# Kernel optimization log

Measured on AMD Instinct MI355X. Metric: run time of the kernel, lower is better.

The kernel has to match this reference:

```python
import jax, jax.numpy as jnp
import numpy as np
from jax import lax

T, D, NH, CATS = 1024, 2048, 2048, 1000


def setup_inputs() -> dict:
    key = jax.random.key(0)
    ks = jax.random.split(key, 16)
    s = 0.02
    return {
        "x": jax.random.normal(ks[0], (T, D), dtype=jnp.float32),
        "Wh": jax.random.normal(ks[1], (NH, D), dtype=jnp.float32) * s,
        "Wz": jax.random.normal(ks[2], (NH, D), dtype=jnp.float32) * s,
        "Wr": jax.random.normal(ks[3], (NH, D), dtype=jnp.float32) * s,
        "Uh": jax.random.normal(ks[4], (NH, NH), dtype=jnp.float32) * s,
        "Uz": jax.random.normal(ks[5], (NH, NH), dtype=jnp.float32) * s,
        "bz": jax.random.normal(ks[6], (NH,), dtype=jnp.float32) * s,
        "Ur": jax.random.normal(ks[7], (NH, NH), dtype=jnp.float32) * s,
        "br": jax.random.normal(ks[8], (NH,), dtype=jnp.float32) * s,
        "Wout": jax.random.normal(ks[9], (CATS, NH), dtype=jnp.float32) * s,
        "h0": jax.random.normal(ks[10], (NH,), dtype=jnp.float32),
        "zt0": jax.random.normal(ks[11], (NH,), dtype=jnp.float32),
        "htilde0": jax.random.normal(ks[12], (NH,), dtype=jnp.float32),
        "hprev0": jax.random.normal(ks[13], (NH,), dtype=jnp.float32),
    }


def reference(x, Wh, Wz, Wr, Uh, Uz, bz, Ur, br, Wout, h0, zt0, htilde0, hprev0):
    # Batch the input projections over all timesteps: [T,d] @ [d,nh] -> [T,nh]
    xh = x @ Wh.T
    xz = x @ Wz.T
    xr = x @ Wr.T

    # Faithful to the original update ORDER: h is computed from the *stale*
    # zt/htilde (from the previous iteration), then gates are refreshed.
    # The original's hadamard(a, b) = linear(a, diag(b)) is exactly a * b.
    def step(carry, xs):
        h, zt, htilde, hprev = carry
        xh_t, xz_t, xr_t = xs
        h_new = (1.0 - zt) * hprev + zt * htilde
        zt_new = jax.nn.sigmoid(xz_t + hprev @ Uz.T + bz)
        htilde_new = jnp.tanh(xh_t + hprev @ Uh.T)
        # rt = sigmoid(xr_t + hprev @ Ur.T + br)  # computed in original, never used
        return (h_new, zt_new, htilde_new, h_new), None

    (h_fin, _, _, _), _ = lax.scan(step, (h0, zt0, htilde0, hprev0), (xh, xz, xr))
    logits = h_fin @ Wout.T  # [cats]
    return jax.nn.softmax(logits, axis=0)
```

## Files before the change

### kernel.cpp

```cpp
#include <hip/hip_runtime.h>
#include <math.h>

#define TT  1024
#define DD  2048
#define NHH 2048
#define CC  1000

__global__ __launch_bounds__(256) void k_gemm(const float* __restrict__ X,
                                              const float* __restrict__ Wh,
                                              const float* __restrict__ Wz,
                                              const float* __restrict__ bz,
                                              float* __restrict__ XH,
                                              float* __restrict__ XZ) {
    __shared__ float As[32][68];
    __shared__ float Bs[32][68];
    const int z = blockIdx.z;
    const float* __restrict__ W = z ? Wz : Wh;
    float* __restrict__ OUT = z ? XZ : XH;
    const int n0 = blockIdx.x * 64;
    const int m0 = blockIdx.y * 64;
    const int tid = threadIdx.x;
    const int tx = tid & 15, ty = tid >> 4;
    const int lr = tid >> 2;
    const int lc = (tid & 3) * 8;

    float acc[4][4] = {};
    for (int k0 = 0; k0 < DD; k0 += 32) {
        float4 a0 = *(const float4*)&X[(size_t)(m0 + lr) * DD + k0 + lc];
        float4 a1 = *(const float4*)&X[(size_t)(m0 + lr) * DD + k0 + lc + 4];
        float4 b0 = *(const float4*)&W[(size_t)(n0 + lr) * DD + k0 + lc];
        float4 b1 = *(const float4*)&W[(size_t)(n0 + lr) * DD + k0 + lc + 4];
        As[lc+0][lr]=a0.x; As[lc+1][lr]=a0.y; As[lc+2][lr]=a0.z; As[lc+3][lr]=a0.w;
        As[lc+4][lr]=a1.x; As[lc+5][lr]=a1.y; As[lc+6][lr]=a1.z; As[lc+7][lr]=a1.w;
        Bs[lc+0][lr]=b0.x; Bs[lc+1][lr]=b0.y; Bs[lc+2][lr]=b0.z; Bs[lc+3][lr]=b0.w;
        Bs[lc+4][lr]=b1.x; Bs[lc+5][lr]=b1.y; Bs[lc+6][lr]=b1.z; Bs[lc+7][lr]=b1.w;
        __syncthreads();
#pragma unroll
        for (int kk = 0; kk < 32; ++kk) {
            float4 av = *(const float4*)&As[kk][ty * 4];
            float4 bv = *(const float4*)&Bs[kk][tx * 4];
            acc[0][0] = fmaf(av.x, bv.x, acc[0][0]); acc[0][1] = fmaf(av.x, bv.y, acc[0][1]);
            acc[0][2] = fmaf(av.x, bv.z, acc[0][2]); acc[0][3] = fmaf(av.x, bv.w, acc[0][3]);
            acc[1][0] = fmaf(av.y, bv.x, acc[1][0]); acc[1][1] = fmaf(av.y, bv.y, acc[1][1]);
            acc[1][2] = fmaf(av.y, bv.z, acc[1][2]); acc[1][3] = fmaf(av.y, bv.w, acc[1][3]);
            acc[2][0] = fmaf(av.z, bv.x, acc[2][0]); acc[2][1] = fmaf(av.z, bv.y, acc[2][1]);
            acc[2][2] = fmaf(av.z, bv.z, acc[2][2]); acc[2][3] = fmaf(av.z, bv.w, acc[2][3]);
            acc[3][0] = fmaf(av.w, bv.x, acc[3][0]); acc[3][1] = fmaf(av.w, bv.y, acc[3][1]);
            acc[3][2] = fmaf(av.w, bv.z, acc[3][2]); acc[3][3] = fmaf(av.w, bv.w, acc[3][3]);
        }
        __syncthreads();
    }
    float4 bias = make_float4(0.f, 0.f, 0.f, 0.f);
    if (z) bias = *(const float4*)&bz[n0 + tx * 4];
#pragma unroll
    for (int i = 0; i < 4; ++i) {
        float4 o = make_float4(acc[i][0] + bias.x, acc[i][1] + bias.y,
                               acc[i][2] + bias.z, acc[i][3] + bias.w);
        *(float4*)&OUT[(size_t)(m0 + ty * 4 + i) * NHH + n0 + tx * 4] = o;
    }
}

__global__ __launch_bounds__(256, 1) void k_recur(
    const float* __restrict__ XH, const float* __restrict__ XZ,
    const float* __restrict__ Uh, const float* __restrict__ Uz,
    const float* __restrict__ zt0, const float* __restrict__ ht0,
    const float* __restrict__ hp0,
    unsigned long long* __restrict__ Hbuf) {
    __shared__ float Hs[NHH];
    __shared__ float dot_s[16];
    const int tid  = threadIdx.x;
    const int wave = tid >> 6, lane = tid & 63;
    const int base8 = blockIdx.x * 8;

    const float* __restrict__ Um = (wave < 2) ? Uz : Uh;
    const int r0 = base8 + (wave & 1) * 4;
    float u[4][32];
#pragma unroll
    for (int r = 0; r < 4; ++r) {
        const float* __restrict__ row = Um + (size_t)(r0 + r) * NHH;
#pragma unroll
        for (int c = 0; c < 8; ++c) {
            float4 v = *(const float4*)&row[c * 256 + lane * 4];
            u[r][c*4+0] = v.x; u[r][c*4+1] = v.y; u[r][c*4+2] = v.z; u[r][c*4+3] = v.w;
        }
    }
#pragma unroll
    for (int k = 0; k < 8; ++k) Hs[k * 256 + tid] = hp0[k * 256 + tid];

    float p_cur = 0.f;
    if (tid < 8) {
        float z0 = zt0[base8 + tid], g0 = ht0[base8 + tid], p0 = hp0[base8 + tid];
        p_cur = (1.0f - z0) * p0 + z0 * g0;
        unsigned long long pr = (1ull << 32) | (unsigned long long)__float_as_uint(p_cur);
        __hip_atomic_store(&Hbuf[(size_t)1 * NHH + base8 + tid], pr,
                           __ATOMIC_RELAXED, __HIP_MEMORY_SCOPE_AGENT);
    }
    __syncthreads();

    for (int t = 1; t < TT; ++t) {
        const unsigned long long* __restrict__ src = Hbuf + (size_t)(t & 3) * NHH;
        unsigned long long pv[8];
#pragma unroll
        for (int k = 0; k < 8; ++k)
            pv[k] = __hip_atomic_load(&src[k * 256 + tid], __ATOMIC_RELAXED, __HIP_MEMORY_SCOPE_AGENT);
        float xzv = 0.f, xhv = 0.f;
        if (tid < 8) {
            xzv = XZ[(size_t)(t - 1) * NHH + base8 + tid];
            xhv = XH[(size_t)(t - 1) * NHH + base8 + tid];
        }
        float a0 = 0.f, a1 = 0.f, a2 = 0.f, a3 = 0.f;
#pragma unroll
        for (int c = 0; c < 8; ++c) {
            float4 h4 = *(const float4*)&Hs[c * 256 + lane * 4];
            a0 = fmaf(u[0][c*4+0], h4.x, fmaf(u[0][c*4+1], h4.y, fmaf(u[0][c*4+2], h4.z, fmaf(u[0][c*4+3], h4.w, a0))));
            a1 = fmaf(u[1][c*4+0], h4.x, fmaf(u[1][c*4+1], h4.y, fmaf(u[1][c*4+2], h4.z, fmaf(u[1][c*4+3], h4.w, a1))));
            a2 = fmaf(u[2][c*4+0], h4.x, fmaf(u[2][c*4+1], h4.y, fmaf(u[2][c*4+2], h4.z, fmaf(u[2][c*4+3], h4.w, a2))));
            a3 = fmaf(u[3][c*4+0], h4.x, fmaf(u[3][c*4+1], h4.y, fmaf(u[3][c*4+2], h4.z, fmaf(u[3][c*4+3], h4.w, a3))));
        }
#pragma unroll
        for (int off = 32; off > 0; off >>= 1) {
            a0 += __shfl_xor(a0, off);
            a1 += __shfl_xor(a1, off);
            a2 += __shfl_xor(a2, off);
            a3 += __shfl_xor(a3, off);
        }
        if (lane == 0) {
            int di = ((wave & 1) * 4) + ((wave >> 1) * 8);
            dot_s[di + 0] = a0; dot_s[di + 1] = a1; dot_s[di + 2] = a2; dot_s[di + 3] = a3;
        }
        __syncthreads();
        if (tid < 8) {
            float z = 1.0f / (1.0f + expf(-(xzv + dot_s[tid])));
            float g = tanhf(xhv + dot_s[8 + tid]);
            float pn = (1.0f - z) * p_cur + z * g;
            p_cur = pn;
            unsigned long long pr = ((unsigned long long)(unsigned)(t + 1) << 32)
                                  | (unsigned long long)__float_as_uint(pn);
            __hip_atomic_store(&Hbuf[(size_t)((t + 1) & 3) * NHH + base8 + tid], pr,
                               __ATOMIC_RELAXED, __HIP_MEMORY_SCOPE_AGENT);
        }
        for (;;) {
            unsigned stale = 0;
#pragma unroll
            for (int k = 0; k < 8; ++k)
                if ((unsigned)(pv[k] >> 32) != (unsigned)t) stale |= (1u << k);
            if (!stale) break;
#pragma unroll
            for (int k = 0; k < 8; ++k)
                if (stale & (1u << k))
                    pv[k] = __hip_atomic_load(&src[k * 256 + tid], __ATOMIC_RELAXED, __HIP_MEMORY_SCOPE_AGENT);
        }
#pragma unroll
        for (int k = 0; k < 8; ++k) Hs[k * 256 + tid] = __uint_as_float((unsigned)pv[k]);
        __syncthreads();
    }
}

__global__ __launch_bounds__(256) void k_logits(const unsigned long long* __restrict__ Hbuf,
                                                const float* __restrict__ Wout,
                                                float* __restrict__ lg) {
    __shared__ float Hs[NHH];
    const int tid = threadIdx.x;
    for (int k = tid; k < NHH; k += 256) Hs[k] = __uint_as_float((unsigned)Hbuf[k]);
    __syncthreads();
    const int wave = tid >> 6, lane = tid & 63;
    const int row = blockIdx.x * 4 + wave;
    float a = 0.f;
#pragma unroll
    for (int c = 0; c < 8; ++c) {
        float4 w = *(const float4*)&Wout[(size_t)row * NHH + c * 256 + lane * 4];
        float4 h = *(const float4*)&Hs[c * 256 + lane * 4];
        a = fmaf(w.x, h.x, fmaf(w.y, h.y, fmaf(w.z, h.z, fmaf(w.w, h.w, a))));
    }
#pragma unroll
    for (int off = 32; off > 0; off >>= 1) a += __shfl_xor(a, off);
    if (lane == 0) lg[row] = a;
}

__global__ __launch_bounds__(1024) void k_softmax(const float* __restrict__ lg,
                                                  float* __restrict__ out) {
    const int i = threadIdx.x;
    __shared__ float red[16];
    __shared__ float bc[2];
    float v = (i < CC) ? lg[i] : -3.0e38f;
    float m = v;
#pragma unroll
    for (int off = 32; off > 0; off >>= 1) m = fmaxf(m, __shfl_xor(m, off));
    if ((i & 63) == 0) red[i >> 6] = m;
    __syncthreads();
    if (i == 0) { float mm = red[0]; for (int k = 1; k < 16; ++k) mm = fmaxf(mm, red[k]); bc[0] = mm; }
    __syncthreads();
    float e = (i < CC) ? expf(v - bc[0]) : 0.f;
    float s = e;
#pragma unroll
    for (int off = 32; off > 0; off >>= 1) s += __shfl_xor(s, off);
    if ((i & 63) == 0) red[i >> 6] = s;
    __syncthreads();
    if (i == 0) { float ss = 0.f; for (int k = 0; k < 16; ++k) ss += red[k]; bc[1] = ss; }
    __syncthreads();
    if (i < CC) out[i] = e / bc[1];
}

extern "C" void kernel_launch(void* const* d_in, const int* in_sizes, int n_in,
                              void* d_out, int out_size, void* d_ws, size_t ws_size,
                              hipStream_t stream) {
    const float* x    = (const float*)d_in[0];
    const float* Wh   = (const float*)d_in[1];
    const float* Wz   = (const float*)d_in[2];
    const float* Uh   = (const float*)d_in[4];
    const float* Uz   = (const float*)d_in[5];
    const float* bz   = (const float*)d_in[6];
    const float* Wout = (const float*)d_in[9];
    const float* zt0  = (const float*)d_in[11];
    const float* ht0  = (const float*)d_in[12];
    const float* hp0  = (const float*)d_in[13];
    float* out = (float*)d_out;

    float* XH = (float*)d_ws;
    float* XZ = XH + (size_t)TT * NHH;
    unsigned long long* Hbuf = (unsigned long long*)(XZ + (size_t)TT * NHH);
    float* lg = (float*)(Hbuf + 4 * NHH);

    k_gemm<<<dim3(NHH / 64, TT / 64, 2), dim3(256), 0, stream>>>(x, Wh, Wz, bz, XH, XZ);
    k_recur<<<dim3(256), dim3(256), 0, stream>>>(XH, XZ, Uh, Uz, zt0, ht0, hp0, Hbuf);
    k_logits<<<dim3(250), dim3(256), 0, stream>>>(Hbuf, Wout, lg);
    k_softmax<<<dim3(1), dim3(1024), 0, stream>>>(lg, out);
}
```

Baseline: 2.044 ms.

## Restructure recurrence: one row per wave, double-buffered LDS, counter sync

The recurrent kernel now launches 512 threads per block with one wave per hidden unit. Each wave holds both its Uz and Uh rows in registers, reduces both dots itself and applies the gate update in lane 0. This removes the shared dot_s stage and both per-step __syncthreads. Hidden state is double-buffered in LDS, and waves sync through an LDS atomic fill counter instead of a block barrier. A new init kernel pre-fills Hbuf with invalid tags, so stale values from earlier runs cannot be mistaken for current ones. The cost is more waves spinning on LDS and global memory, plus higher register pressure.

```diff
diff --git a/kernel.cpp b/kernel.cpp
--- a/kernel.cpp
+++ b/kernel.cpp
@@ -5,6 +5,14 @@
 #define DD  2048
 #define NHH 2048
 #define CC  1000
+
+#define LDS_LOAD_ACQ(P)  __hip_atomic_load((P), __ATOMIC_ACQUIRE, __HIP_MEMORY_SCOPE_WORKGROUP)
+#define LDS_ADD_REL(P)   __hip_atomic_fetch_add((P), 1, __ATOMIC_RELEASE, __HIP_MEMORY_SCOPE_WORKGROUP)
+
+__global__ void k_init(unsigned long long* __restrict__ Hbuf) {
+    int i = blockIdx.x * blockDim.x + threadIdx.x;
+    if (i < 4 * NHH) Hbuf[i] = 0xFFFFFFFF00000000ull;
+}
 
 __global__ __launch_bounds__(256) void k_gemm(const float* __restrict__ X,
                                               const float* __restrict__ Wh,
@@ -60,100 +68,107 @@
     }
 }
 
-__global__ __launch_bounds__(256, 1) void k_recur(
+__global__ __launch_bounds__(512) void k_recur(
     const float* __restrict__ XH, const float* __restrict__ XZ,
     const float* __restrict__ Uh, const float* __restrict__ Uz,
     const float* __restrict__ zt0, const float* __restrict__ ht0,
     const float* __restrict__ hp0,
     unsigned long long* __restrict__ Hbuf) {
-    __shared__ float Hs[NHH];
-    __shared__ float dot_s[16];
+    __shared__ float Hs[2][NHH];
+    __shared__ int fill_cnt;
     const int tid  = threadIdx.x;
     const int wave = tid >> 6, lane = tid & 63;
     const int base8 = blockIdx.x * 8;
-
-    const float* __restrict__ Um = (wave < 2) ? Uz : Uh;
-    const int r0 = base8 + (wave & 1) * 4;
-    float u[4][32];
-#pragma unroll
-    for (int r = 0; r < 4; ++r) {
-        const float* __restrict__ row = Um + (size_t)(r0 + r) * NHH;
-#pragma unroll
-        for (int c = 0; c < 8; ++c) {
-            float4 v = *(const float4*)&row[c * 256 + lane * 4];
-            u[r][c*4+0] = v.x; u[r][c*4+1] = v.y; u[r][c*4+2] = v.z; u[r][c*4+3] = v.w;
-        }
-    }
-#pragma unroll
-    for (int k = 0; k < 8; ++k) Hs[k * 256 + tid] = hp0[k * 256 + tid];
-
-    float p_cur = 0.f;
-    if (tid < 8) {
-        float z0 = zt0[base8 + tid], g0 = ht0[base8 + tid], p0 = hp0[base8 + tid];
-        p_cur = (1.0f - z0) * p0 + z0 * g0;
-        unsigned long long pr = (1ull << 32) | (unsigned long long)__float_as_uint(p_cur);
-        __hip_atomic_store(&Hbuf[(size_t)1 * NHH + base8 + tid], pr,
+    const int j = base8 + wave;
+
+    const float* __restrict__ rz = Uz + (size_t)j * NHH + lane * 4;
+    const float* __restrict__ rh = Uh + (size_t)j * NHH + lane * 4;
+    float4 uz0 = *(const float4*)&rz[0 * 256];
+    float4 uz1 = *(const float4*)&rz[1 * 256];
+    float4 uz2 = *(const float4*)&rz[2 * 256];
+    float4 uz3 = *(const float4*)&rz[3 * 256];
+    float4 uz4 = *(const float4*)&rz[4 * 256];
+    float4 uz5 = *(const float4*)&rz[5 * 256];
+    float4 uz6 = *(const float4*)&rz[6 * 256];
+    float4 uz7 = *(const float4*)&rz[7 * 256];
+    float4 uh0 = *(const float4*)&rh[0 * 256];
+    float4 uh1 = *(const float4*)&rh[1 * 256];
+    float4 uh2 = *(const float4*)&rh[2 * 256];
+    float4 uh3 = *(const float4*)&rh[3 * 256];
+    float4 uh4 = *(const float4*)&rh[4 * 256];
+    float4 uh5 = *(const float4*)&rh[5 * 256];
+    float4 uh6 = *(const float4*)&rh[6 * 256];
+    float4 uh7 = *(const float4*)&rh[7 * 256];
+
+    if (tid == 0) fill_cnt = 0;
+    *(float4*)&Hs[0][tid * 4] = *(const float4*)&hp0[tid * 4];
+
+    float p = 0.f, xz_cur = 0.f, xh_cur = 0.f;
+    if (lane == 0) {
+        float z0 = zt0[j], g0 = ht0[j], p0 = hp0[j];
+        p = (1.0f - z0) * p0 + z0 * g0;
+        unsigned long long pr = (1ull << 32) | (unsigned long long)__float_as_uint(p);
+        __hip_atomic_store(&Hbuf[(size_t)1 * NHH + j], pr,
                            __ATOMIC_RELAXED, __HIP_MEMORY_SCOPE_AGENT);
-    }
-    __syncthreads();
+        xz_cur = XZ[j];
+        xh_cur = XH[j];
+    }
+    __syncthreads();
+
+#define MVSTEP(C) { \
+        float4 h4 = *(const float4*)&HA[(C) * 256 + lane * 4]; \
+        az = fmaf(uz##C.x, h4.x, fmaf(uz##C.y, h4.y, fmaf(uz##C.z, h4.z, fmaf(uz##C.w, h4.w, az)))); \
+        ah = fmaf(uh##C.x, h4.x, fmaf(uh##C.y, h4.y, fmaf(uh##C.z, h4.z, fmaf(uh##C.w, h4.w, ah)))); }
 
     for (int t = 1; t < TT; ++t) {
         const unsigned long long* __restrict__ src = Hbuf + (size_t)(t & 3) * NHH;
-        unsigned long long pv[8];
-#pragma unroll
-        for (int k = 0; k < 8; ++k)
-            pv[k] = __hip_atomic_load(&src[k * 256 + tid], __ATOMIC_RELAXED, __HIP_MEMORY_SCOPE_AGENT);
-        float xzv = 0.f, xhv = 0.f;
-        if (tid < 8) {
-            xzv = XZ[(size_t)(t - 1) * NHH + base8 + tid];
-            xhv = XH[(size_t)(t - 1) * NHH + base8 + tid];
-        }
-        float a0 = 0.f, a1 = 0.f, a2 = 0.f, a3 = 0.f;
-#pragma unroll
-        for (int c = 0; c < 8; ++c) {
-            float4 h4 = *(const float4*)&Hs[c * 256 + lane * 4];
-            a0 = fmaf(u[0][c*4+0], h4.x, fmaf(u[0][c*4+1], h4.y, fmaf(u[0][c*4+2], h4.z, fmaf(u[0][c*4+3], h4.w, a0))));
-            a1 = fmaf(u[1][c*4+0], h4.x, fmaf(u[1][c*4+1], h4.y, fmaf(u[1][c*4+2], h4.z, fmaf(u[1][c*4+3], h4.w, a1))));
-            a2 = fmaf(u[2][c*4+0], h4.x, fmaf(u[2][c*4+1], h4.y, fmaf(u[2][c*4+2], h4.z, fmaf(u[2][c*4+3], h4.w, a2))));
-            a3 = fmaf(u[3][c*4+0], h4.x, fmaf(u[3][c*4+1], h4.y, fmaf(u[3][c*4+2], h4.z, fmaf(u[3][c*4+3], h4.w, a3))));
-        }
-#pragma unroll
-        for (int off = 32; off > 0; off >>= 1) {
-            a0 += __shfl_xor(a0, off);
-            a1 += __shfl_xor(a1, off);
-            a2 += __shfl_xor(a2, off);
-            a3 += __shfl_xor(a3, off);
+        unsigned long long pv0 = __hip_atomic_load(&src[0 * 512 + tid], __ATOMIC_RELAXED, __HIP_MEMORY_SCOPE_AGENT);
+        unsigned long long pv1 = __hip_atomic_load(&src[1 * 512 + tid], __ATOMIC_RELAXED, __HIP_MEMORY_SCOPE_AGENT);
+        unsigned long long pv2 = __hip_atomic_load(&src[2 * 512 + tid], __ATOMIC_RELAXED, __HIP_MEMORY_SCOPE_AGENT);
+        unsigned long long pv3 = __hip_atomic_load(&src[3 * 512 + tid], __ATOMIC_RELAXED, __HIP_MEMORY_SCOPE_AGENT);
+        if (t > 1)
+            while (LDS_LOAD_ACQ(&fill_cnt) < 8 * (t - 1)) __builtin_amdgcn_s_sleep(0);
+        const float* __restrict__ HA = Hs[(t - 1) & 1];
+        float az = 0.f, ah = 0.f;
+        MVSTEP(0) MVSTEP(1) MVSTEP(2) MVSTEP(3)
+        MVSTEP(4) MVSTEP(5) MVSTEP(6) MVSTEP(7)
+#pragma unroll
+        for (int off = 1; off <= 32; off <<= 1) {
+            az += __shfl_xor(az, off);
+            ah += __shfl_xor(ah, off);
         }
         if (lane == 0) {
-            int di = ((wave & 1) * 4) + ((wave >> 1) * 8);
-            dot_s[di + 0] = a0; dot_s[di + 1] = a1; dot_s[di + 2] = a2; dot_s[di + 3] = a3;
-        }
-        __syncthreads();
-        if (tid < 8) {
-            float z = 1.0f / (1.0f + expf(-(xzv + dot_s[tid])));
-            float g = tanhf(xhv + dot_s[8 + tid]);
-            float pn = (1.0f - z) * p_cur + z * g;
-            p_cur = pn;
+            float z = 1.0f / (1.0f + expf(-(xz_cur + az)));
+            float g = tanhf(xh_cur + ah);
+            p = (1.0f - z) * p + z * g;
             unsigned long long pr = ((unsigned long long)(unsigned)(t + 1) << 32)
-                                  | (unsigned long long)__float_as_uint(pn);
-            __hip_atomic_store(&Hbuf[(size_t)((t + 1) & 3) * NHH + base8 + tid], pr,
+                                  | (unsigned long long)__float_as_uint(p);
+            __hip_atomic_store(&Hbuf[(size_t)((t + 1) & 3) * NHH + j], pr,
                                __ATOMIC_RELAXED, __HIP_MEMORY_SCOPE_AGENT);
+            xz_cur = XZ[(size_t)t * NHH + j];
+            xh_cur = XH[(size_t)t * NHH + j];
         }
         for (;;) {
             unsigned stale = 0;
-#pragma unroll
-            for (int k = 0; k < 8; ++k)
-                if ((unsigned)(pv[k] >> 32) != (unsigned)t) stale |= (1u << k);
+            if ((unsigned)(pv0 >> 32) != (unsigned)t) stale |= 1u;
+            if ((unsigned)(pv1 >> 32) != (unsigned)t) stale |= 2u;
+            if ((unsigned)(pv2 >> 32) != (unsigned)t) stale |= 4u;
+            if ((unsigned)(pv3 >> 32) != (unsigned)t) stale |= 8u;
             if (!stale) break;
-#pragma unroll
-            for (int k = 0; k < 8; ++k)
-                if (stale & (1u << k))
-                    pv[k] = __hip_atomic_load(&src[k * 256 + tid], __ATOMIC_RELAXED, __HIP_MEMORY_SCOPE_AGENT);
-        }
-#pragma unroll
-        for (int k = 0; k < 8; ++k) Hs[k * 256 + tid] = __uint_as_float((unsigned)pv[k]);
-        __syncthreads();
-    }
+            __builtin_amdgcn_s_sleep(1);
+            if (stale & 1u) pv0 = __hip_atomic_load(&src[0 * 512 + tid], __ATOMIC_RELAXED, __HIP_MEMORY_SCOPE_AGENT);
+            if (stale & 2u) pv1 = __hip_atomic_load(&src[1 * 512 + tid], __ATOMIC_RELAXED, __HIP_MEMORY_SCOPE_AGENT);
+            if (stale & 4u) pv2 = __hip_atomic_load(&src[2 * 512 + tid], __ATOMIC_RELAXED, __HIP_MEMORY_SCOPE_AGENT);
+            if (stale & 8u) pv3 = __hip_atomic_load(&src[3 * 512 + tid], __ATOMIC_RELAXED, __HIP_MEMORY_SCOPE_AGENT);
+        }
+        float* __restrict__ HB = Hs[t & 1];
+        HB[0 * 512 + tid] = __uint_as_float((unsigned)pv0);
+        HB[1 * 512 + tid] = __uint_as_float((unsigned)pv1);
+        HB[2 * 512 + tid] = __uint_as_float((unsigned)pv2);
+        HB[3 * 512 + tid] = __uint_as_float((unsigned)pv3);
+        if (lane == 63) LDS_ADD_REL(&fill_cnt);
+    }
+#undef MVSTEP
 }
 
 __global__ __launch_bounds__(256) void k_logits(const unsigned long long* __restrict__ Hbuf,
@@ -221,8 +236,9 @@
     unsigned long long* Hbuf = (unsigned long long*)(XZ + (size_t)TT * NHH);
     float* lg = (float*)(Hbuf + 4 * NHH);
 
+    k_init<<<dim3((4 * NHH + 255) / 256), dim3(256), 0, stream>>>(Hbuf);
     k_gemm<<<dim3(NHH / 64, TT / 64, 2), dim3(256), 0, stream>>>(x, Wh, Wz, bz, XH, XZ);
-    k_recur<<<dim3(256), dim3(256), 0, stream>>>(XH, XZ, Uh, Uz, zt0, ht0, hp0, Hbuf);
+    k_recur<<<dim3(256), dim3(512), 0, stream>>>(XH, XZ, Uh, Uz, zt0, ht0, hp0, Hbuf);
     k_logits<<<dim3(250), dim3(256), 0, stream>>>(Hbuf, Wout, lg);
     k_softmax<<<dim3(1), dim3(1024), 0, stream>>>(lg, out);
 }
```

New measurement: 2.754 ms. 34.8% more time.
